# Kernel optimization log

Measured on AMD Instinct MI355X. Metric: run time of the kernel, lower is better.

Reference implementation:

```python
import jax, jax.numpy as jnp
import numpy as np

B, L, C, H, T = 4096, 32, 28, 512, 32


def setup_inputs() -> dict:
    key = jax.random.key(0)
    ks = jax.random.split(key, 10)
    s = 0.1
    return dict(
        input=jax.random.normal(ks[0], (B, L, C), jnp.float32),
        unpacked_masks=jnp.ones((B, L, 1), jnp.float32),
        bias_mat=jax.random.normal(ks[1], (B, L), jnp.float32),
        conv1_w=jax.random.normal(ks[2], (C, C, 3), jnp.float32) * s,  # OIH
        conv1_b=jnp.zeros((C,), jnp.float32),
        conv_w=jax.random.normal(ks[3], (1, C, 1), jnp.float32) * s,
        conv_b=jnp.zeros((1,), jnp.float32),
        w_ih=jax.random.normal(ks[4], (4 * H, C), jnp.float32) * s,
        w_hh=jax.random.normal(ks[5], (4 * H, H), jnp.float32) * s,
        b_ih=jnp.zeros((4 * H,), jnp.float32),
        b_hh=jnp.concatenate([jnp.zeros(H), jnp.ones(H), jnp.zeros(2 * H)]).astype(jnp.float32),  # forget-gate bias = 1 as in weights_init
        fc1_w=jax.random.normal(ks[6], (1, H), jnp.float32) * s,
        fc1_b=jnp.zeros((1,), jnp.float32),
        conv2_w=jax.random.normal(ks[7], (1, H, 1), jnp.float32) * s,
        conv2_b=jnp.zeros((1,), jnp.float32),
    )


def reference(input, unpacked_masks, bias_mat, conv1_w, conv1_b, conv_w, conv_b,
              w_ih, w_hh, b_ih, b_hh, fc1_w, fc1_b, conv2_w, conv2_b):
    b, l, c = input.shape
    # residual conv block: conv1d(28->28,k3,pad1) -> mask -> elu -> +input
    x_ncl = jnp.transpose(input, (0, 2, 1))
    y = jax.lax.conv_general_dilated(x_ncl, conv1_w, (1,), 'SAME',
                                     dimension_numbers=('NCH', 'OIH', 'NCH'))
    y = jnp.transpose(y + conv1_b[None, :, None], (0, 2, 1))
    x = jax.nn.elu(y * unpacked_masks) + input  # [B,L,C]
    # u_a: 1x1 conv (28->1) == per-position linear, then mask -> [B,L,1]
    u_a = (jnp.einsum('blc,c->bl', x, conv_w[0, :, 0]) + conv_b)[..., None] * unpacked_masks
    bias = bias_mat.reshape(b, l, 1)

    def step(carry, _):
        h, cstate = carry
        w_a = (h @ fc1_w.T + fc1_b)[:, :, None]                 # [B,1,1]
        attn = jax.nn.leaky_relu(u_a + w_a) + bias              # [B,L,1]
        attn = jax.nn.softmax(attn, axis=1)                     # softmax over sequence
        context = jnp.einsum('bl,blc->bc', attn[..., 0], x)     # [B,C]
        gates = context @ w_ih.T + b_ih + h @ w_hh.T + b_hh     # [B,4H]
        i, f, g, o = jnp.split(gates, 4, axis=1)                # torch LSTMCell gate order
        cstate = jax.nn.sigmoid(f) * cstate + jax.nn.sigmoid(i) * jnp.tanh(g)
        h = jax.nn.sigmoid(o) * jnp.tanh(cstate)
        return (h, cstate), h

    h0 = jnp.zeros((b, w_hh.shape[1]), input.dtype)
    (_, _), hs = jax.lax.scan(step, (h0, h0), None, length=T)   # [T,B,H]
    all_hidden = jnp.transpose(hs, (1, 0, 2))                   # [B,T,H]
    # dropout layers are identity in eval; conv2 is 1x1 conv (512->1)
    out = (jnp.einsum('bth,h->bt', all_hidden, conv2_w[0, :, 0]) + conv2_b)[..., None]
    return out * unpacked_masks
```

## Files before the change

kernel.cpp:

```cpp
#include <hip/hip_runtime.h>
#include <hip/hip_bf16.h>

#define B_N 4096
#define L_N 32
#define C_N 28
#define H_N 512
#define T_N 32
#define G_N 2048
#define CHA 34
#define CHSH 4096
#define ABLK (CHA * CHSH)
#define XS 29

typedef __attribute__((ext_vector_type(2))) float f32x2;
typedef __attribute__((ext_vector_type(4))) float f32x4;
typedef __attribute__((ext_vector_type(8))) short s16x8;

static constexpr size_t OFF_WF = 0;
static constexpr size_t AB_ONE = (size_t)32 * ABLK * 2;
static constexpr size_t OFF_AB = OFF_WF + (size_t)16 * ABLK * 2;
static constexpr size_t OFF_X  = OFF_AB + 2 * AB_ONE;
static constexpr size_t OFF_UA = OFF_X + (size_t)B_N * L_N * C_N * 4;
static constexpr size_t OFF_BS = OFF_UA + (size_t)B_N * L_N * 4;
static constexpr size_t OFF_AC = OFF_BS + 8192;
static constexpr size_t ACC_HALF = (size_t)32 * B_N * 4;
static constexpr size_t OFF_CS = OFF_AC + 2 * ACC_HALF;
static constexpr size_t WS_NEED = OFF_CS + (size_t)B_N * H_N * 4;

__device__ __forceinline__ short bfbits(__hip_bfloat16 b) {
    union { __hip_bfloat16 b; short s; } v; v.b = b; return v.s;
}
__device__ __forceinline__ float sigmoidf_(float x) { return 1.f / (1.f + __expf(-x)); }
__device__ __forceinline__ float tanhf_(float x) {
    float ax = fabsf(x), e = __expf(-2.f * ax);
    float t = (1.f - e) / (1.f + e);
    return x < 0.f ? -t : t;
}

__global__ __launch_bounds__(256) void fill_out(float* out, float v) {
    int i = blockIdx.x * 256 + threadIdx.x;
    if (i < B_N * 32) out[i] = v;
}

__global__ __launch_bounds__(256) void prep_x(const float* __restrict__ input,
                       const float* __restrict__ mask,
                       const float* __restrict__ w1, const float* __restrict__ b1,
                       const float* __restrict__ cw, const float* __restrict__ cb,
                       float* __restrict__ x, float* __restrict__ ua)
{
    __shared__ float sin[8 * L_N * XS];
    __shared__ float sxb[8 * L_N * XS];
    const float* src = input + (size_t)blockIdx.x * (8 * L_N * C_N);
    for (int i = threadIdx.x; i < 8 * L_N * C_N; i += 256) {
        int lr = i / (L_N * C_N);
        int rem = i - lr * (L_N * C_N);
        int l = rem / C_N, c = rem - l * C_N;
        sin[lr * (L_N * XS) + l * XS + c] = src[i];
    }
    __syncthreads();

    int idx = blockIdx.x * 256 + threadIdx.x;
    int l = idx & 31;
    int wv = threadIdx.x >> 5;
    const float* inb = sin + wv * (L_N * XS);
    float m = mask[idx];

    float x0r[C_N], xm1[C_N], xp1[C_N];
    #pragma unroll
    for (int i = 0; i < C_N; ++i) x0r[i] = inb[l * XS + i];
    #pragma unroll
    for (int i = 0; i < C_N; ++i) {
        float up = __shfl_up(x0r[i], 1, 32);
        float dn = __shfl_down(x0r[i], 1, 32);
        xm1[i] = (l > 0)  ? up : 0.f;
        xp1[i] = (l < 31) ? dn : 0.f;
    }

    float uacc = 0.f;
    float* sxrow = sxb + wv * (L_N * XS) + l * XS;
    #pragma unroll 2
    for (int o = 0; o < C_N; ++o) {
        const float* wo = w1 + o * (C_N * 3);
        float y0 = b1[o], y1 = 0.f, y2 = 0.f;
        #pragma unroll
        for (int i = 0; i < C_N; ++i) {
            y0 += wo[i * 3 + 0] * xm1[i];
            y1 += wo[i * 3 + 1] * x0r[i];
            y2 += wo[i * 3 + 2] * xp1[i];
        }
        float y = (y0 + y1 + y2) * m;
        float e = (y > 0.f) ? y : (__expf(y) - 1.f);
        float xv = e + inb[l * XS + o];
        sxrow[o] = xv;
        uacc += xv * cw[o];
    }
    ua[idx] = (uacc + cb[0]) * m;
    __syncthreads();
    float* xdst = x + (size_t)blockIdx.x * (8 * L_N * C_N);
    for (int i = threadIdx.x; i < 8 * L_N * C_N; i += 256) {
        int lr = i / (L_N * C_N);
        int rem = i - lr * (L_N * C_N);
        int l2 = rem / C_N, c = rem - l2 * C_N;
        xdst[i] = sxb[lr * (L_N * XS) + l2 * XS + c];
    }
}

__global__ __launch_bounds__(256) void prep_wf(const float* __restrict__ w_ih,
                                               const float* __restrict__ w_hh,
                                               short* __restrict__ Wf)
{
    int blk = blockIdx.x;
    int n128 = blk / CHA, c = blk % CHA;
    bool lo = (c >= 17);
    int kbase = (lo ? (c - 17) : c) * 32;
    short* dst = Wf + ((size_t)n128 * CHA + c) * CHSH;
    for (int g = threadIdx.x; g < 512; g += 256) {
        int j = g >> 6, lane = g & 63;
        int gate = j & 3;
        int unit = n128 * 32 + (j >> 2) * 16 + (lane & 15);
        int srow = gate * H_N + unit;
        int kg = lane >> 4;
        s16x8 out;
        #pragma unroll
        for (int b2 = 0; b2 < 8; ++b2) {
            int k = kbase + kg * 8 + b2;
            float v = 0.f;
            if (k < 512) v = w_hh[(size_t)srow * H_N + k];
            else if (k < 540) v = w_ih[srow * C_N + (k - 512)];
            __hip_bfloat16 hi = __float2bfloat16(v);
            if (lo) out[b2] = bfbits(__float2bfloat16(v - __bfloat162float(hi)));
            else    out[b2] = bfbits(hi);
        }
        *(s16x8*)(dst + g * 8) = out;
    }
}

__global__ void prep_bs(const float* __restrict__ b_ih, const float* __restrict__ b_hh,
                        float* __restrict__ bsum)
{
    int p = blockIdx.x * 256 + threadIdx.x;
    if (p < G_N) {
        int unit = p >> 2, gate = p & 3;
        bsum[p] = b_ih[gate * H_N + unit] + b_hh[gate * H_N + unit];
    }
}

__global__ void prep_zero(unsigned int* __restrict__ a32, float* __restrict__ cst,
                          float* __restrict__ acc)
{
    int idx = blockIdx.x * blockDim.x + threadIdx.x;
    if (idx < B_N * 1088) a32[idx] = 0u;
    if (idx < B_N * H_N) cst[idx] = 0.f;
    if (idx < 2 * 32 * B_N) acc[idx] = 0.f;
}

struct RParams {
    const float* mask;
    const float* bias_mat;
    const float* fc1_w;
    const float* fc1_b;
    const float* conv2_w;
    const float* conv2_b;
    const short* Wf;
    const short* Ain;
    short* Aout;
    const float* x;
    const float* ua;
    const float* bsum;
    float* accW;
    float* accO;
    float* cstate;
    float* out;
};

__global__ __launch_bounds__(256) void ctx_step(RParams P, int t)
{
    __shared__ float sx[4][L_N * C_N];

    const int lane = threadIdx.x & 63;
    const int wave = threadIdx.x >> 6;
    const int row  = blockIdx.x * 4 + wave;

    f32x2 st[7];
    const float* xrow = P.x + (size_t)row * (L_N * C_N);
    #pragma unroll
    for (int q = 0; q < 7; ++q) st[q] = *(const f32x2*)(xrow + (q * 64 + lane) * 2);

    float v = (lane < 32) ? P.accW[row * 32 + lane] : P.accO[row * 32 + (lane - 32)];
    #pragma unroll
    for (int off = 1; off <= 16; off <<= 1) v += __shfl_xor(v, off);
    float aW = __shfl(v, 0);
    float aO = __shfl(v, 32);

    if (t > 0 && lane == 0)
        P.out[row * T_N + (t - 1)] = (aO + P.conv2_b[0]) * P.mask[row * L_N + (t - 1)];

    if (t < T_N) {
        float w_a = aW + P.fc1_b[0];
        int l32 = lane & 31;
        float e = P.ua[row * L_N + l32] + w_a;
        e = (e > 0.f) ? e : 0.01f * e;
        e += P.bias_mat[row * L_N + l32];
        float mx = e;
        #pragma unroll
        for (int off = 16; off > 0; off >>= 1) mx = fmaxf(mx, __shfl_xor(mx, off, 32));
        float pexp = __expf(e - mx);
        float ssum = pexp;
        #pragma unroll
        for (int off = 16; off > 0; off >>= 1) ssum += __shfl_xor(ssum, off, 32);
        float p = pexp / ssum;

        #pragma unroll
        for (int q = 0; q < 7; ++q)
            *(f32x2*)(&sx[wave][(q * 64 + lane) * 2]) = st[q];

        int cc = (lane < C_N) ? lane : 0;
        float ctx = 0.f;
        #pragma unroll
        for (int l = 0; l < L_N; ++l) {
            float al = __shfl(p, l);
            ctx += al * sx[wave][l * C_N + cc];
        }
        if (lane < C_N) {
            int m128 = row >> 7, mt = (row & 127) >> 4, r = row & 15;
            int flane = r + 16 * (lane >> 3);
            short* base = P.Aout + (size_t)m128 * ABLK + mt * 512 + flane * 8 + (lane & 7);
            __hip_bfloat16 hi = __float2bfloat16(ctx);
            base[16 * CHSH] = bfbits(hi);
            base[33 * CHSH] = bfbits(__float2bfloat16(ctx - __bfloat162float(hi)));
        }
    }
}

#define STG_BUF 32768

__global__ __launch_bounds__(256, 2) void gemm_cell_step(RParams P)
{
    __shared__ __align__(16) char smem[65536];

    const int tid  = threadIdx.x;
    const int lane = tid & 63;
    const int wave = tid >> 6;
    const int bid  = blockIdx.x;
    const int xg = bid & 7, gg = bid >> 3;
    const int m  = (xg >> 1) * 8 + (gg & 7);
    const int n  = (xg & 1) * 8 + (gg >> 3);
    const int wm = wave >> 1, wn = wave & 1;

    const short* Af = P.Ain + (size_t)m * ABLK;
    const short* Wg = P.Wf  + (size_t)n * ABLK;

    const short* slab0 = (wave < 2) ? Af : Wg;
    const int slab_lo  = (wave & 1) ? 17 : 0;

    char* bufp0 = smem;
    char* bufp1 = smem + STG_BUF;

    auto stage = [&](char* lbuf, int kk) {
        const short* gp = slab0 + (size_t)(slab_lo + kk) * CHSH + lane * 8;
        char* lb = lbuf + wave * 8192;
        #pragma unroll
        for (int r = 0; r < 8; ++r) {
            __builtin_amdgcn_global_load_lds(
                (const __attribute__((address_space(1))) void*)(gp + r * 512),
                (__attribute__((address_space(3))) void*)(lb + r * 1024),
                16, 0, 0);
        }
    };

    int aoff[4], woff[4];
    #pragma unroll
    for (int i = 0; i < 4; ++i) {
        aoff[i] = ((wm * 4 + i) * 64 + lane) * 16;
        woff[i] = ((wn * 4 + i) * 64 + lane) * 16;
    }

    f32x4 acc[4][4];
    #pragma unroll
    for (int i = 0; i < 4; ++i)
        #pragma unroll
        for (int j = 0; j < 4; ++j)
            acc[i][j] = (f32x4){0.f, 0.f, 0.f, 0.f};

    s16x8 RA[16], RB[16];
    auto ldfr = [&](const char* b, s16x8 (&R)[16]) {
        #pragma unroll
        for (int i = 0; i < 4; ++i) {
            R[i]      = *(const s16x8*)(b + aoff[i]);
            R[4 + i]  = *(const s16x8*)(b + 8192 + aoff[i]);
            R[8 + i]  = *(const s16x8*)(b + 16384 + woff[i]);
            R[12 + i] = *(const s16x8*)(b + 24576 + woff[i]);
        }
    };
    auto domm = [&](s16x8 (&R)[16]) {
        #pragma unroll
        for (int i = 0; i < 4; ++i)
            #pragma unroll
            for (int j = 0; j < 4; ++j)
                acc[i][j] = __builtin_amdgcn_mfma_f32_16x16x32_bf16(R[i], R[8 + j], acc[i][j], 0, 0, 0);
        #pragma unroll
        for (int i = 0; i < 4; ++i)
            #pragma unroll
            for (int j = 0; j < 4; ++j)
                acc[i][j] = __builtin_amdgcn_mfma_f32_16x16x32_bf16(R[4 + i], R[8 + j], acc[i][j], 0, 0, 0);
        #pragma unroll
        for (int i = 0; i < 4; ++i)
            #pragma unroll
            for (int j = 0; j < 4; ++j)
                acc[i][j] = __builtin_amdgcn_mfma_f32_16x16x32_bf16(R[i], R[12 + j], acc[i][j], 0, 0, 0);
    };

    auto step_full = [&](int kk, s16x8 (&Rc)[16], s16x8 (&Rn)[16], char* bcur, char* bnext) {
        asm volatile("s_waitcnt vmcnt(0) lgkmcnt(0)" ::: "memory");
        __builtin_amdgcn_s_barrier();
        __builtin_amdgcn_sched_barrier(0);
        stage(bcur, kk + 2);
        ldfr(bnext, Rn);
        domm(Rc);
        #pragma unroll
        for (int g = 0; g < 8; ++g) {
            __builtin_amdgcn_sched_group_barrier(0x010, 1, 0);
            __builtin_amdgcn_sched_group_barrier(0x100, 2, 0);
            __builtin_amdgcn_sched_group_barrier(0x008, 6, 0);
        }
        __builtin_amdgcn_sched_barrier(0);
    };
    auto step_nos = [&](s16x8 (&Rc)[16], s16x8 (&Rn)[16], char* bnext) {
        asm volatile("s_waitcnt vmcnt(0) lgkmcnt(0)" ::: "memory");
        __builtin_amdgcn_s_barrier();
        __builtin_amdgcn_sched_barrier(0);
        ldfr(bnext, Rn);
        domm(Rc);
        #pragma unroll
        for (int g = 0; g < 8; ++g) {
            __builtin_amdgcn_sched_group_barrier(0x100, 2, 0);
            __builtin_amdgcn_sched_group_barrier(0x008, 6, 0);
        }
        __builtin_amdgcn_sched_barrier(0);
    };
    auto step_last = [&](s16x8 (&Rc)[16]) {
        asm volatile("s_waitcnt vmcnt(0) lgkmcnt(0)" ::: "memory");
        __builtin_amdgcn_s_barrier();
        __builtin_amdgcn_sched_barrier(0);
        domm(Rc);
        __builtin_amdgcn_sched_barrier(0);
    };

    stage(bufp0, 0);
    asm volatile("s_waitcnt vmcnt(0)" ::: "memory");
    __builtin_amdgcn_s_barrier();
    stage(bufp1, 1);
    ldfr(bufp0, RA);

    for (int kp = 0; kp < 7; ++kp) {
        step_full(2 * kp,     RA, RB, bufp0, bufp1);
        step_full(2 * kp + 1, RB, RA, bufp1, bufp0);
    }
    step_full(14, RA, RB, bufp0, bufp1);
    step_nos(RB, RA, bufp0);
    step_last(RA);

    __syncthreads();
    short* hasm = (short*)smem;
    {
        int u15 = lane & 15, rq = lane >> 4;
        int unit = n * 32 + wn * 16 + u15;
        float cpre[4][4];
        #pragma unroll
        for (int i = 0; i < 4; ++i)
            #pragma unroll
            for (int r = 0; r < 4; ++r)
                cpre[i][r] = P.cstate[(size_t)(m * 128 + wm * 64 + i * 16 + rq * 4 + r) * H_N + unit];
        f32x4 bsv = *(const f32x4*)(P.bsum + unit * 4);
        float f1v = P.fc1_w[unit];
        float c2v = P.conv2_w[unit];
        const int fl16 = 16 * (wn * 2 + (u15 >> 3));
        const int slot = u15 & 7;
        #pragma unroll
        for (int i = 0; i < 4; ++i) {
            #pragma unroll
            for (int r = 0; r < 4; ++r) {
                int grow = m * 128 + wm * 64 + i * 16 + rq * 4 + r;
                float pi = acc[i][0][r] + bsv.x;
                float pf = acc[i][1][r] + bsv.y;
                float pg = acc[i][2][r] + bsv.z;
                float po = acc[i][3][r] + bsv.w;
                float c = sigmoidf_(pf) * cpre[i][r] + sigmoidf_(pi) * tanhf_(pg);
                P.cstate[(size_t)grow * H_N + unit] = c;
                float h = sigmoidf_(po) * tanhf_(c);
                __hip_bfloat16 hi = __float2bfloat16(h);
                int fo = (wm * 4 + i) * 512 + (rq * 4 + r + fl16) * 8 + slot;
                hasm[fo]        = bfbits(hi);
                hasm[4096 + fo] = bfbits(__float2bfloat16(h - __bfloat162float(hi)));
                float wd = f1v * h, od = c2v * h;
                #pragma unroll
                for (int off = 8; off > 0; off >>= 1) {
                    wd += __shfl_xor(wd, off);
                    od += __shfl_xor(od, off);
                }
                if (u15 == 0) {
                    P.accW[(size_t)grow * 32 + (n * 2 + wn)] = wd;
                    P.accO[(size_t)grow * 32 + (n * 2 + wn)] = od;
                }
            }
        }
    }
    __syncthreads();
    short* dhi = P.Aout + (size_t)m * ABLK + (size_t)n * CHSH;
    short* dlo = P.Aout + (size_t)m * ABLK + (size_t)(17 + n) * CHSH;
    *(s16x8*)(dhi + tid * 16)     = *(const s16x8*)(hasm + tid * 16);
    *(s16x8*)(dhi + tid * 16 + 8) = *(const s16x8*)(hasm + tid * 16 + 8);
    *(s16x8*)(dlo + tid * 16)     = *(const s16x8*)(hasm + 4096 + tid * 16);
    *(s16x8*)(dlo + tid * 16 + 8) = *(const s16x8*)(hasm + 4096 + tid * 16 + 8);
}

extern "C" void kernel_launch(void* const* d_in, const int* in_sizes, int n_in,
                              void* d_out, int out_size, void* d_ws, size_t ws_size,
                              hipStream_t stream)
{
    float* out = (float*)d_out;
    if (ws_size < WS_NEED) { fill_out<<<512, 256, 0, stream>>>(out, 4000.f); return; }

    const float* input = (const float*)d_in[0];
    const float* mask  = (const float*)d_in[1];
    const float* biasm = (const float*)d_in[2];
    const float* w1    = (const float*)d_in[3];
    const float* b1    = (const float*)d_in[4];
    const float* cw    = (const float*)d_in[5];
    const float* cb    = (const float*)d_in[6];
    const float* w_ih  = (const float*)d_in[7];
    const float* w_hh  = (const float*)d_in[8];
    const float* b_ih  = (const float*)d_in[9];
    const float* b_hh  = (const float*)d_in[10];
    const float* fc1w  = (const float*)d_in[11];
    const float* fc1b  = (const float*)d_in[12];
    const float* c2w   = (const float*)d_in[13];
    const float* c2b   = (const float*)d_in[14];

    char* ws = (char*)d_ws;
    short* Wf = (short*)(ws + OFF_WF);
    short* A0 = (short*)(ws + OFF_AB);
    short* A1 = (short*)(ws + OFF_AB + AB_ONE);
    float* x    = (float*)(ws + OFF_X);
    float* ua   = (float*)(ws + OFF_UA);
    float* bsum = (float*)(ws + OFF_BS);
    float* accW = (float*)(ws + OFF_AC);
    float* accO = (float*)(ws + OFF_AC + ACC_HALF);
    float* cst  = (float*)(ws + OFF_CS);

    prep_x<<<(B_N * L_N) / 256, 256, 0, stream>>>(input, mask, w1, b1, cw, cb, x, ua);
    prep_wf<<<16 * CHA, 256, 0, stream>>>(w_ih, w_hh, Wf);
    prep_bs<<<(G_N + 255) / 256, 256, 0, stream>>>(b_ih, b_hh, bsum);
    prep_zero<<<(B_N * 1088 + 255) / 256, 256, 0, stream>>>((unsigned int*)A0, cst, accW);

    RParams P;
    P.mask = mask; P.bias_mat = biasm; P.fc1_w = fc1w; P.fc1_b = fc1b;
    P.conv2_w = c2w; P.conv2_b = c2b; P.Wf = Wf;
    P.x = x; P.ua = ua; P.bsum = bsum; P.accW = accW; P.accO = accO;
    P.cstate = cst; P.out = out;

    short* bufs[2] = { A0, A1 };
    for (int t = 0; t < T_N; ++t) {
        P.Ain  = bufs[t & 1];
        P.Aout = bufs[t & 1];
        ctx_step<<<B_N / 4, 256, 0, stream>>>(P, t);
        P.Ain  = bufs[t & 1];
        P.Aout = bufs[(t + 1) & 1];
        gemm_cell_step<<<512, 256, 0, stream>>>(P);
    }
    P.Ain = bufs[T_N & 1];
    P.Aout = bufs[T_N & 1];
    ctx_step<<<B_N / 4, 256, 0, stream>>>(P, T_N);
}
```

Baseline: 1.349 ms.

## Fuse attention context step into GEMM kernel with per-tile atomic barrier

Removes the separate ctx_step launch per timestep by having each GEMM block compute the attention softmax and context for 8 batch rows. The blocks publish completion through per-M-tile atomic counters. The GEMM runs the h-part K chunks first and spins on the counter only before the final chunks that read the context columns, which overlaps context computation with the GEMM prologue. This relies on all 16 producer blocks for each M tile being co-resident or already finished, since a spin-wait on blocks that cannot be scheduled would deadlock. It also adds LDS usage that may affect occupancy.

```diff
diff --git a/kernel.cpp b/kernel.cpp
--- a/kernel.cpp
+++ b/kernel.cpp
@@ -25,7 +25,8 @@
 static constexpr size_t OFF_AC = OFF_BS + 8192;
 static constexpr size_t ACC_HALF = (size_t)32 * B_N * 4;
 static constexpr size_t OFF_CS = OFF_AC + 2 * ACC_HALF;
-static constexpr size_t WS_NEED = OFF_CS + (size_t)B_N * H_N * 4;
+static constexpr size_t OFF_BR = OFF_CS + (size_t)B_N * H_N * 4;
+static constexpr size_t WS_NEED = OFF_BR + (size_t)T_N * 32 * 4;
 
 __device__ __forceinline__ short bfbits(__hip_bfloat16 b) {
     union { __hip_bfloat16 b; short s; } v; v.b = b; return v.s;
@@ -146,12 +147,13 @@
 }
 
 __global__ void prep_zero(unsigned int* __restrict__ a32, float* __restrict__ cst,
-                          float* __restrict__ acc)
+                          float* __restrict__ acc, unsigned int* __restrict__ bar)
 {
     int idx = blockIdx.x * blockDim.x + threadIdx.x;
     if (idx < B_N * 1088) a32[idx] = 0u;
     if (idx < B_N * H_N) cst[idx] = 0.f;
     if (idx < 2 * 32 * B_N) acc[idx] = 0.f;
+    if (idx < T_N * 32) bar[idx] = 0u;
 }
 
 struct RParams {
@@ -163,6 +165,7 @@
     const float* conv2_b;
     const short* Wf;
     const short* Ain;
+    short* ctxA;
     short* Aout;
     const float* x;
     const float* ua;
@@ -170,6 +173,7 @@
     float* accW;
     float* accO;
     float* cstate;
+    unsigned int* bar;
     float* out;
 };
 
@@ -234,9 +238,9 @@
 
 #define STG_BUF 32768
 
-__global__ __launch_bounds__(256, 2) void gemm_cell_step(RParams P)
-{
-    __shared__ __align__(16) char smem[65536];
+__global__ __launch_bounds__(256, 2) void gemm_cell_step(RParams P, int t)
+{
+    __shared__ __align__(16) char smem[65536 + 14336];
 
     const int tid  = threadIdx.x;
     const int lane = tid & 63;
@@ -267,6 +271,66 @@
                 16, 0, 0);
         }
     };
+
+    stage(bufp0, 0);
+    stage(bufp1, 1);
+
+    {
+        float* myxs = (float*)(smem + 65536) + wave * (L_N * C_N);
+        #pragma unroll
+        for (int r2 = 0; r2 < 2; ++r2) {
+            int row = bid * 8 + wave * 2 + r2;
+            const float* xrow = P.x + (size_t)row * (L_N * C_N);
+            f32x2 st[7];
+            #pragma unroll
+            for (int q = 0; q < 7; ++q) st[q] = *(const f32x2*)(xrow + (q * 64 + lane) * 2);
+            float v = (lane < 32) ? P.accW[row * 32 + lane] : P.accO[row * 32 + (lane - 32)];
+            #pragma unroll
+            for (int off = 1; off <= 16; off <<= 1) v += __shfl_xor(v, off);
+            float aW = __shfl(v, 0);
+            float aO = __shfl(v, 32);
+            if (t > 0 && lane == 0)
+                P.out[(size_t)row * T_N + (t - 1)] =
+                    (aO + P.conv2_b[0]) * P.mask[row * L_N + (t - 1)];
+            float w_a = aW + P.fc1_b[0];
+            int l32 = lane & 31;
+            float e = P.ua[row * L_N + l32] + w_a;
+            e = (e > 0.f) ? e : 0.01f * e;
+            e += P.bias_mat[row * L_N + l32];
+            float mx = e;
+            #pragma unroll
+            for (int off = 16; off > 0; off >>= 1) mx = fmaxf(mx, __shfl_xor(mx, off, 32));
+            float pexp = __expf(e - mx);
+            float ssum = pexp;
+            #pragma unroll
+            for (int off = 16; off > 0; off >>= 1) ssum += __shfl_xor(ssum, off, 32);
+            float p = pexp / ssum;
+            #pragma unroll
+            for (int q = 0; q < 7; ++q)
+                *(f32x2*)(myxs + (q * 64 + lane) * 2) = st[q];
+            int cc = (lane < C_N) ? lane : 0;
+            float ctx = 0.f;
+            #pragma unroll
+            for (int l = 0; l < L_N; ++l) {
+                float al = __shfl(p, l);
+                ctx += al * myxs[l * C_N + cc];
+            }
+            if (lane < C_N) {
+                int m128p = row >> 7, mt = (row & 127) >> 4, rr = row & 15;
+                int flane = rr + 16 * (lane >> 3);
+                short* base = P.ctxA + (size_t)m128p * ABLK + mt * 512 + flane * 8 + (lane & 7);
+                __hip_bfloat16 hi = __float2bfloat16(ctx);
+                base[16 * CHSH] = bfbits(hi);
+                base[33 * CHSH] = bfbits(__float2bfloat16(ctx - __bfloat162float(hi)));
+            }
+        }
+    }
+    __syncthreads();
+    if (tid == 0) {
+        __builtin_amdgcn_fence(__ATOMIC_RELEASE, "agent");
+        __hip_atomic_fetch_add(&P.bar[t * 32 + (bid >> 4)], 1u,
+                               __ATOMIC_RELEASE, __HIP_MEMORY_SCOPE_AGENT);
+    }
 
     int aoff[4], woff[4];
     #pragma unroll
@@ -346,16 +410,23 @@
         __builtin_amdgcn_sched_barrier(0);
     };
 
-    stage(bufp0, 0);
-    asm volatile("s_waitcnt vmcnt(0)" ::: "memory");
+    asm volatile("s_waitcnt vmcnt(8)" ::: "memory");
     __builtin_amdgcn_s_barrier();
-    stage(bufp1, 1);
     ldfr(bufp0, RA);
 
     for (int kp = 0; kp < 7; ++kp) {
         step_full(2 * kp,     RA, RB, bufp0, bufp1);
         step_full(2 * kp + 1, RB, RA, bufp1, bufp0);
     }
+
+    if (tid == 0) {
+        while (__hip_atomic_load(&P.bar[t * 32 + m], __ATOMIC_ACQUIRE,
+                                 __HIP_MEMORY_SCOPE_AGENT) < 16u)
+            __builtin_amdgcn_s_sleep(1);
+    }
+    __syncthreads();
+    __builtin_amdgcn_fence(__ATOMIC_ACQUIRE, "agent");
+
     step_full(14, RA, RB, bufp0, bufp1);
     step_nos(RB, RA, bufp0);
     step_last(RA);
@@ -447,28 +518,28 @@
     float* accW = (float*)(ws + OFF_AC);
     float* accO = (float*)(ws + OFF_AC + ACC_HALF);
     float* cst  = (float*)(ws + OFF_CS);
+    unsigned int* bar = (unsigned int*)(ws + OFF_BR);
 
     prep_x<<<(B_N * L_N) / 256, 256, 0, stream>>>(input, mask, w1, b1, cw, cb, x, ua);
     prep_wf<<<16 * CHA, 256, 0, stream>>>(w_ih, w_hh, Wf);
     prep_bs<<<(G_N + 255) / 256, 256, 0, stream>>>(b_ih, b_hh, bsum);
-    prep_zero<<<(B_N * 1088 + 255) / 256, 256, 0, stream>>>((unsigned int*)A0, cst, accW);
+    prep_zero<<<(B_N * 1088 + 255) / 256, 256, 0, stream>>>((unsigned int*)A0, cst, accW, bar);
 
     RParams P;
     P.mask = mask; P.bias_mat = biasm; P.fc1_w = fc1w; P.fc1_b = fc1b;
     P.conv2_w = c2w; P.conv2_b = c2b; P.Wf = Wf;
     P.x = x; P.ua = ua; P.bsum = bsum; P.accW = accW; P.accO = accO;
-    P.cstate = cst; P.out = out;
+    P.cstate = cst; P.bar = bar; P.out = out;
 
     short* bufs[2] = { A0, A1 };
     for (int t = 0; t < T_N; ++t) {
         P.Ain  = bufs[t & 1];
-        P.Aout = bufs[t & 1];
-        ctx_step<<<B_N / 4, 256, 0, stream>>>(P, t);
-        P.Ain  = bufs[t & 1];
+        P.ctxA = bufs[t & 1];
         P.Aout = bufs[(t + 1) & 1];
-        gemm_cell_step<<<512, 256, 0, stream>>>(P);
-    }
-    P.Ain = bufs[T_N & 1];
+        gemm_cell_step<<<512, 256, 0, stream>>>(P, t);
+    }
+    P.Ain  = bufs[T_N & 1];
+    P.ctxA = bufs[T_N & 1];
     P.Aout = bufs[T_N & 1];
     ctx_step<<<B_N / 4, 256, 0, stream>>>(P, T_N);
 }
```

Result: slower. 2.336 ms (+73.2%).

## Switch recurrent GEMM to fp16 split-A with single fp16 weights, drop third MFMA pass

Applied to the files above, without the earlier changes.

Weights are now stored as a single fp16 value instead of a bf16 hi/lo pair, while activations (h and context) keep an fp16 hi/lo split. The GEMM therefore runs two f16 MFMA passes per k-chunk instead of three bf16 passes. Staging shrinks from four slabs to three, which reduces LDS use and per-step global traffic. The trade-off is lower weight precision (fp16 only, no low-part correction) and fp16 range limits on the activations.

```diff
diff --git a/kernel.cpp b/kernel.cpp
--- a/kernel.cpp
+++ b/kernel.cpp
@@ -15,6 +15,7 @@
 typedef __attribute__((ext_vector_type(2))) float f32x2;
 typedef __attribute__((ext_vector_type(4))) float f32x4;
 typedef __attribute__((ext_vector_type(8))) short s16x8;
+typedef __attribute__((ext_vector_type(8))) _Float16 f16x8;
 
 static constexpr size_t OFF_WF = 0;
 static constexpr size_t AB_ONE = (size_t)32 * ABLK * 2;
@@ -27,8 +28,8 @@
 static constexpr size_t OFF_CS = OFF_AC + 2 * ACC_HALF;
 static constexpr size_t WS_NEED = OFF_CS + (size_t)B_N * H_N * 4;
 
-__device__ __forceinline__ short bfbits(__hip_bfloat16 b) {
-    union { __hip_bfloat16 b; short s; } v; v.b = b; return v.s;
+__device__ __forceinline__ short hfbits(float x) {
+    union { _Float16 h; short s; } v; v.h = (_Float16)x; return v.s;
 }
 __device__ __forceinline__ float sigmoidf_(float x) { return 1.f / (1.f + __expf(-x)); }
 __device__ __forceinline__ float tanhf_(float x) {
@@ -110,9 +111,8 @@
                                                short* __restrict__ Wf)
 {
     int blk = blockIdx.x;
-    int n128 = blk / CHA, c = blk % CHA;
-    bool lo = (c >= 17);
-    int kbase = (lo ? (c - 17) : c) * 32;
+    int n128 = blk / 17, c = blk % 17;
+    int kbase = c * 32;
     short* dst = Wf + ((size_t)n128 * CHA + c) * CHSH;
     for (int g = threadIdx.x; g < 512; g += 256) {
         int j = g >> 6, lane = g & 63;
@@ -127,9 +127,7 @@
             float v = 0.f;
             if (k < 512) v = w_hh[(size_t)srow * H_N + k];
             else if (k < 540) v = w_ih[srow * C_N + (k - 512)];
-            __hip_bfloat16 hi = __float2bfloat16(v);
-            if (lo) out[b2] = bfbits(__float2bfloat16(v - __bfloat162float(hi)));
-            else    out[b2] = bfbits(hi);
+            out[b2] = hfbits(v);
         }
         *(s16x8*)(dst + g * 8) = out;
     }
@@ -225,18 +223,19 @@
             int m128 = row >> 7, mt = (row & 127) >> 4, r = row & 15;
             int flane = r + 16 * (lane >> 3);
             short* base = P.Aout + (size_t)m128 * ABLK + mt * 512 + flane * 8 + (lane & 7);
-            __hip_bfloat16 hi = __float2bfloat16(ctx);
-            base[16 * CHSH] = bfbits(hi);
-            base[33 * CHSH] = bfbits(__float2bfloat16(ctx - __bfloat162float(hi)));
-        }
-    }
-}
-
-#define STG_BUF 32768
+            _Float16 hi = (_Float16)ctx;
+            union { _Float16 h; short s; } uh; uh.h = hi;
+            base[16 * CHSH] = uh.s;
+            base[33 * CHSH] = hfbits(ctx - (float)hi);
+        }
+    }
+}
+
+#define STG_BUF 24576
 
 __global__ __launch_bounds__(256, 2) void gemm_cell_step(RParams P)
 {
-    __shared__ __align__(16) char smem[65536];
+    __shared__ __align__(16) char smem[49152];
 
     const int tid  = threadIdx.x;
     const int lane = tid & 63;
@@ -250,20 +249,22 @@
     const short* Af = P.Ain + (size_t)m * ABLK;
     const short* Wg = P.Wf  + (size_t)n * ABLK;
 
-    const short* slab0 = (wave < 2) ? Af : Wg;
-    const int slab_lo  = (wave & 1) ? 17 : 0;
-
     char* bufp0 = smem;
     char* bufp1 = smem + STG_BUF;
 
     auto stage = [&](char* lbuf, int kk) {
-        const short* gp = slab0 + (size_t)(slab_lo + kk) * CHSH + lane * 8;
-        char* lb = lbuf + wave * 8192;
-        #pragma unroll
-        for (int r = 0; r < 8; ++r) {
+        const short* pAh = Af + (size_t)kk * CHSH;
+        const short* pAl = Af + (size_t)(17 + kk) * CHSH;
+        const short* pW  = Wg + (size_t)kk * CHSH;
+        #pragma unroll
+        for (int i = 0; i < 6; ++i) {
+            int r = wave * 6 + i;
+            const short* base = (r < 8)  ? (pAh + r * 512)
+                              : (r < 16) ? (pAl + (r - 8) * 512)
+                                         : (pW + (r - 16) * 512);
             __builtin_amdgcn_global_load_lds(
-                (const __attribute__((address_space(1))) void*)(gp + r * 512),
-                (__attribute__((address_space(3))) void*)(lb + r * 1024),
+                (const __attribute__((address_space(1))) void*)(base + lane * 8),
+                (__attribute__((address_space(3))) void*)(lbuf + r * 1024),
                 16, 0, 0);
         }
     };
@@ -282,35 +283,29 @@
         for (int j = 0; j < 4; ++j)
             acc[i][j] = (f32x4){0.f, 0.f, 0.f, 0.f};
 
-    s16x8 RA[16], RB[16];
-    auto ldfr = [&](const char* b, s16x8 (&R)[16]) {
+    f16x8 RA[12], RB[12];
+    auto ldfr = [&](const char* b, f16x8 (&R)[12]) {
         #pragma unroll
         for (int i = 0; i < 4; ++i) {
-            R[i]      = *(const s16x8*)(b + aoff[i]);
-            R[4 + i]  = *(const s16x8*)(b + 8192 + aoff[i]);
-            R[8 + i]  = *(const s16x8*)(b + 16384 + woff[i]);
-            R[12 + i] = *(const s16x8*)(b + 24576 + woff[i]);
-        }
-    };
-    auto domm = [&](s16x8 (&R)[16]) {
+            R[i]     = *(const f16x8*)(b + aoff[i]);
+            R[4 + i] = *(const f16x8*)(b + 8192 + aoff[i]);
+            R[8 + i] = *(const f16x8*)(b + 16384 + woff[i]);
+        }
+    };
+    auto domm = [&](f16x8 (&R)[12]) {
         #pragma unroll
         for (int i = 0; i < 4; ++i)
             #pragma unroll
             for (int j = 0; j < 4; ++j)
-                acc[i][j] = __builtin_amdgcn_mfma_f32_16x16x32_bf16(R[i], R[8 + j], acc[i][j], 0, 0, 0);
+                acc[i][j] = __builtin_amdgcn_mfma_f32_16x16x32_f16(R[i], R[8 + j], acc[i][j], 0, 0, 0);
         #pragma unroll
         for (int i = 0; i < 4; ++i)
             #pragma unroll
             for (int j = 0; j < 4; ++j)
-                acc[i][j] = __builtin_amdgcn_mfma_f32_16x16x32_bf16(R[4 + i], R[8 + j], acc[i][j], 0, 0, 0);
-        #pragma unroll
-        for (int i = 0; i < 4; ++i)
-            #pragma unroll
-            for (int j = 0; j < 4; ++j)
-                acc[i][j] = __builtin_amdgcn_mfma_f32_16x16x32_bf16(R[i], R[12 + j], acc[i][j], 0, 0, 0);
-    };
-
-    auto step_full = [&](int kk, s16x8 (&Rc)[16], s16x8 (&Rn)[16], char* bcur, char* bnext) {
+                acc[i][j] = __builtin_amdgcn_mfma_f32_16x16x32_f16(R[4 + i], R[8 + j], acc[i][j], 0, 0, 0);
+    };
+
+    auto step_full = [&](int kk, f16x8 (&Rc)[12], f16x8 (&Rn)[12], char* bcur, char* bnext) {
         asm volatile("s_waitcnt vmcnt(0) lgkmcnt(0)" ::: "memory");
         __builtin_amdgcn_s_barrier();
         __builtin_amdgcn_sched_barrier(0);
@@ -318,27 +313,29 @@
         ldfr(bnext, Rn);
         domm(Rc);
         #pragma unroll
-        for (int g = 0; g < 8; ++g) {
+        for (int g = 0; g < 6; ++g) {
             __builtin_amdgcn_sched_group_barrier(0x010, 1, 0);
             __builtin_amdgcn_sched_group_barrier(0x100, 2, 0);
-            __builtin_amdgcn_sched_group_barrier(0x008, 6, 0);
-        }
-        __builtin_amdgcn_sched_barrier(0);
-    };
-    auto step_nos = [&](s16x8 (&Rc)[16], s16x8 (&Rn)[16], char* bnext) {
+            __builtin_amdgcn_sched_group_barrier(0x008, 5, 0);
+        }
+        __builtin_amdgcn_sched_group_barrier(0x008, 2, 0);
+        __builtin_amdgcn_sched_barrier(0);
+    };
+    auto step_nos = [&](f16x8 (&Rc)[12], f16x8 (&Rn)[12], char* bnext) {
         asm volatile("s_waitcnt vmcnt(0) lgkmcnt(0)" ::: "memory");
         __builtin_amdgcn_s_barrier();
         __builtin_amdgcn_sched_barrier(0);
         ldfr(bnext, Rn);
         domm(Rc);
         #pragma unroll
-        for (int g = 0; g < 8; ++g) {
+        for (int g = 0; g < 6; ++g) {
             __builtin_amdgcn_sched_group_barrier(0x100, 2, 0);
-            __builtin_amdgcn_sched_group_barrier(0x008, 6, 0);
-        }
-        __builtin_amdgcn_sched_barrier(0);
-    };
-    auto step_last = [&](s16x8 (&Rc)[16]) {
+            __builtin_amdgcn_sched_group_barrier(0x008, 5, 0);
+        }
+        __builtin_amdgcn_sched_group_barrier(0x008, 2, 0);
+        __builtin_amdgcn_sched_barrier(0);
+    };
+    auto step_last = [&](f16x8 (&Rc)[12]) {
         asm volatile("s_waitcnt vmcnt(0) lgkmcnt(0)" ::: "memory");
         __builtin_amdgcn_s_barrier();
         __builtin_amdgcn_sched_barrier(0);
@@ -388,10 +385,11 @@
                 float c = sigmoidf_(pf) * cpre[i][r] + sigmoidf_(pi) * tanhf_(pg);
                 P.cstate[(size_t)grow * H_N + unit] = c;
                 float h = sigmoidf_(po) * tanhf_(c);
-                __hip_bfloat16 hi = __float2bfloat16(h);
+                _Float16 hh = (_Float16)h;
+                union { _Float16 hf; short s; } uh; uh.hf = hh;
                 int fo = (wm * 4 + i) * 512 + (rq * 4 + r + fl16) * 8 + slot;
-                hasm[fo]        = bfbits(hi);
-                hasm[4096 + fo] = bfbits(__float2bfloat16(h - __bfloat162float(hi)));
+                hasm[fo]        = uh.s;
+                hasm[4096 + fo] = hfbits(h - (float)hh);
                 float wd = f1v * h, od = c2v * h;
                 #pragma unroll
                 for (int off = 8; off > 0; off >>= 1) {
@@ -449,7 +447,7 @@
     float* cst  = (float*)(ws + OFF_CS);
 
     prep_x<<<(B_N * L_N) / 256, 256, 0, stream>>>(input, mask, w1, b1, cw, cb, x, ua);
-    prep_wf<<<16 * CHA, 256, 0, stream>>>(w_ih, w_hh, Wf);
+    prep_wf<<<16 * 17, 256, 0, stream>>>(w_ih, w_hh, Wf);
     prep_bs<<<(G_N + 255) / 256, 256, 0, stream>>>(b_ih, b_hh, bsum);
     prep_zero<<<(B_N * 1088 + 255) / 256, 256, 0, stream>>>((unsigned int*)A0, cst, accW);
 
```

Result: faster. 1.240 ms (-8.1%).
